# Performance work log

Hardware: AMD Instinct MI355X
Metric: run time of the kernel (lower is better)

The kernel has to match this reference:

```python
import jax, jax.numpy as jnp
import numpy as np

E = 1024          # embed_dim
BUCKET = 16       # bucket_size
TAU = 0.75        # sinkhorn_tau
ITERS = 8         # sinkhorn_iters
SCALE = E ** -0.5


def setup_inputs() -> dict:
    key = jax.random.key(0)
    ks = jax.random.split(key, 12)
    T, S, B = 4096, 4096, 8
    w = 1.0 / np.sqrt(E)  # ~xavier scale
    return {
        "query": jax.random.normal(ks[0], (T, B, E), jnp.float32),
        "key_t": jax.random.normal(ks[1], (S, B, E), jnp.float32),
        "value": jax.random.normal(ks[2], (S, B, E), jnp.float32),
        "key_padding_mask": jnp.zeros((B, S), jnp.bool_),
        "Wq": jax.random.normal(ks[3], (E, E), jnp.float32) * w,
        "bq": jax.random.normal(ks[4], (E,), jnp.float32) * 0.01,
        "Wk": jax.random.normal(ks[5], (E, E), jnp.float32) * w,
        "bk": jax.random.normal(ks[6], (E,), jnp.float32) * 0.01,
        "Wv": jax.random.normal(ks[7], (E, E), jnp.float32) * w,
        "bv": jax.random.normal(ks[8], (E,), jnp.float32) * 0.01,
        "Wo": jax.random.normal(ks[9], (E, E), jnp.float32) * w,
        "bo": jnp.zeros((E,), jnp.float32),
    }


def reference(query, key_t, value, key_padding_mask, Wq, bq, Wk, bk, Wv, bv, Wo, bo):
    # Projections in (T, B, E) layout
    q = query @ Wq.T + bq
    k = key_t @ Wk.T + bk
    v = value @ Wv.T + bv
    # (B, T, E)
    q = jnp.swapaxes(q, 0, 1)
    k = jnp.swapaxes(k, 0, 1)
    v = jnp.swapaxes(v, 0, 1)
    B, T, Ed = q.shape
    S = k.shape[1]
    nb, nkb = T // BUCKET, S // BUCKET  # T,S chosen as exact multiples -> no pad
    # aggregate_buckets: mean-pool q,k; flatten v per bucket
    qb = q.reshape(B, nb, BUCKET, Ed).mean(axis=2)          # (B, nb, E)
    kb = k.reshape(B, nkb, BUCKET, Ed).mean(axis=2)         # (B, nkb, E)
    vb = v.reshape(B, nkb, BUCKET * Ed)                     # (B, nkb, BUCKET*E)
    # key padding mask: bucket is padded iff all positions padded (prod)
    kpm_b = jnp.all(key_padding_mask.reshape(B, nkb, BUCKET), axis=2)  # (B, nkb)
    # energy_fn == 'dot'
    attn = jnp.einsum('bte,bse->bts', qb, kb) * SCALE       # (B, nb, nkb)
    neg_inf = -jnp.finfo(attn.dtype).max
    final_mask = kpm_b[:, None, :] & (~kpm_b)[:, :, None]   # (B, nb, nkb), nb==nkb
    attn = jnp.where(final_mask, neg_inf, attn)
    attn = jnp.where(jnp.swapaxes(final_mask, 1, 2), neg_inf, attn)
    # gumbel_sinkhorn in eval mode (noise_factor=0): log-sinkhorn normalization
    la = attn / TAU
    for _ in range(ITERS):
        la = la - jax.nn.logsumexp(la, axis=-1, keepdims=True)
        la = la - jax.nn.logsumexp(la, axis=-2, keepdims=True)
    p = jnp.exp(la)                                         # (B, nb, nkb)
    # attend over flattened value buckets, then undo bucket aggregation
    out = jnp.einsum('bts,bsf->btf', p, vb)                 # (B, nb, BUCKET*E)
    out = out.reshape(B, nb * BUCKET, Ed)                   # (B, T, E)
    out = jnp.swapaxes(out, 0, 1)                           # (T, B, E)
    return out @ Wo.T + bo
```

## Files before the change

kernel.cpp:

```cpp
#include <hip/hip_runtime.h>


typedef __bf16 bhalf;
typedef __bf16 bh4 __attribute__((ext_vector_type(4)));
typedef __bf16 bh8 __attribute__((ext_vector_type(8)));
typedef float f32x4 __attribute__((ext_vector_type(4)));

__device__ __forceinline__ void async16(const bhalf* g, bhalf* l) {
    __builtin_amdgcn_global_load_lds(
        (const __attribute__((address_space(1))) unsigned int*)g,
        (__attribute__((address_space(3))) unsigned int*)l,
        16, 0, 0);
}

__device__ __forceinline__ void f2b_body(const float* in, bhalf* out, int idx) {
    const float4* p = (const float4*)in + (size_t)idx * 2;
    float4 x = p[0], y = p[1];
    bh8 o;
    o[0] = (bhalf)x.x; o[1] = (bhalf)x.y; o[2] = (bhalf)x.z; o[3] = (bhalf)x.w;
    o[4] = (bhalf)y.x; o[5] = (bhalf)y.y; o[6] = (bhalf)y.z; o[7] = (bhalf)y.w;
    *(bh8*)(out + (size_t)idx * 8) = o;
}

__global__ void f2b_kernel(const float* __restrict__ in, bhalf* __restrict__ out, int n8) {
    int idx = blockIdx.x * 256 + threadIdx.x;
    if (idx < n8) f2b_body(in, out, idx);
}

__global__ void f2b4_kernel(const float* __restrict__ a, const float* __restrict__ b,
                            const float* __restrict__ c, const float* __restrict__ d,
                            bhalf* __restrict__ out) {
    const float* srcs[4] = {a, b, c, d};
    int idx = blockIdx.x * 256 + threadIdx.x;
    f2b_body(srcs[blockIdx.y], out + (size_t)blockIdx.y * 1048576, idx);
}

__global__ void pool2_kernel(const float* __restrict__ q, const float* __restrict__ k,
                             bhalf* __restrict__ oq, bhalf* __restrict__ ok) {
    const float* in = blockIdx.y ? k : q;
    bhalf* out = blockIdx.y ? ok : oq;
    int row = blockIdx.x;
    int b = row >> 8, tb = row & 255;
    int e = threadIdx.x * 4;
    const float* base = in + ((size_t)(tb * 16) * 8 + b) * 1024 + e;
    float sx = 0.f, sy = 0.f, sz = 0.f, sw = 0.f;
#pragma unroll
    for (int i = 0; i < 16; ++i) {
        float4 v = *(const float4*)(base + (size_t)i * 8192);
        sx += v.x; sy += v.y; sz += v.z; sw += v.w;
    }
    bh4 o;
    o[0] = (bhalf)(sx * 0.0625f);
    o[1] = (bhalf)(sy * 0.0625f);
    o[2] = (bhalf)(sz * 0.0625f);
    o[3] = (bhalf)(sw * 0.0625f);
    *(bh4*)(out + (size_t)row * 1024 + e) = o;
}

__global__ __launch_bounds__(256) void gemm_nt(
    const bhalf* __restrict__ A, const bhalf* __restrict__ B,
    void* __restrict__ Cv, const float* __restrict__ bias, const float* __restrict__ bias2,
    int lda, int ldb, long ldc, int K,
    float alpha, int outBf16, int swz,
    long zsA, long zsB, long zsC, unsigned zmaskA)
{
    __shared__ bhalf As[128 * 64];
    __shared__ bhalf Bs[128 * 64];
    unsigned z = blockIdx.z;
    A += (size_t)(z & zmaskA) * zsA;
    B += (size_t)z * zsB;
    if (z == 1 && bias2) bias = bias2;
    long coff = (long)z * zsC;
    int bx = blockIdx.x, by = blockIdx.y;
    if (swz) {
        int linear = by * 8 + bx;
        int xcd = linear & 7, idx = linear >> 3;
        bx = idx & 7;
        by = xcd * ((int)gridDim.y >> 3) + (idx >> 3);
    }
    int m0 = by * 128, n0 = bx * 128;
    int tid = threadIdx.x;
    int w = tid >> 6, lane = tid & 63;
    int quad = lane >> 4, l16 = lane & 15;
    int wm = (w & 1) * 64, wn = (w >> 1) * 64;
    int srow = lane >> 3;
    int sg = (lane & 7) ^ srow;

    f32x4 acc[4][4] = {};

    for (int k0 = 0; k0 < K; k0 += 64) {
#pragma unroll
        for (int j = 0; j < 4; ++j) {
            int blk = j * 4 + w;
            int r = blk * 8 + srow;
            async16(A + (size_t)(m0 + r) * lda + (k0 + sg * 8), &As[blk * 512]);
            async16(B + (size_t)(n0 + r) * ldb + (k0 + sg * 8), &Bs[blk * 512]);
        }
        __syncthreads();
#pragma unroll
        for (int kk = 0; kk < 2; ++kk) {
            bh8 fa[4], fb[4];
            int gsw = (((kk << 2) + quad) ^ (l16 & 7)) * 8;
#pragma unroll
            for (int i = 0; i < 4; ++i) {
                fa[i] = *(const bh8*)&As[(wm + i * 16 + l16) * 64 + gsw];
                fb[i] = *(const bh8*)&Bs[(wn + i * 16 + l16) * 64 + gsw];
            }
#pragma unroll
            for (int i = 0; i < 4; ++i)
#pragma unroll
                for (int j = 0; j < 4; ++j)
                    acc[i][j] = __builtin_amdgcn_mfma_f32_16x16x32_bf16(
                        fa[i], fb[j], acc[i][j], 0, 0, 0);
        }
        __syncthreads();
    }

#pragma unroll
    for (int i = 0; i < 4; ++i) {
        int row = m0 + wm + i * 16 + quad * 4;
#pragma unroll
        for (int j = 0; j < 4; ++j) {
            int col = n0 + wn + j * 16 + l16;
            float bb = bias ? bias[col] : 0.f;
#pragma unroll
            for (int r2 = 0; r2 < 4; ++r2) {
                float v = alpha * acc[i][j][r2] + bb;
                long off = coff + (long)(row + r2) * ldc + col;
                if (outBf16) ((bhalf*)Cv)[off] = (bhalf)v;
                else         ((float*)Cv)[off] = v;
            }
        }
    }
}

__global__ __launch_bounds__(1024) void sinkhorn_kernel(
    const float* __restrict__ la_in, bhalf* __restrict__ p_out)
{
    int b = blockIdx.x;
    const float* A = la_in + (size_t)b * 65536;
    int tid = threadIdx.x;
    int br = tid >> 5, bc = tid & 31;
    int r0 = br * 8, c0 = bc * 8;
    float a[8][8];
#pragma unroll
    for (int r = 0; r < 8; ++r) {
        float4 v0 = *(const float4*)(A + (size_t)(r0 + r) * 256 + c0);
        float4 v1 = *(const float4*)(A + (size_t)(r0 + r) * 256 + c0 + 4);
        a[r][0] = v0.x; a[r][1] = v0.y; a[r][2] = v0.z; a[r][3] = v0.w;
        a[r][4] = v1.x; a[r][5] = v1.y; a[r][6] = v1.z; a[r][7] = v1.w;
    }
    __shared__ float lm[16][256];
    __shared__ float ls[16][256];

    for (int it = 0; it < 8; ++it) {
#pragma unroll
        for (int r = 0; r < 8; ++r) {
            float m = a[r][0];
#pragma unroll
            for (int c = 1; c < 8; ++c) m = fmaxf(m, a[r][c]);
#pragma unroll
            for (int d = 1; d < 32; d <<= 1) m = fmaxf(m, __shfl_xor(m, d, 64));
            float s = 0.f;
#pragma unroll
            for (int c = 0; c < 8; ++c) s += __expf(a[r][c] - m);
#pragma unroll
            for (int d = 1; d < 32; d <<= 1) s += __shfl_xor(s, d, 64);
            float lse = m + __logf(s);
#pragma unroll
            for (int c = 0; c < 8; ++c) a[r][c] -= lse;
        }
        __syncthreads();
#pragma unroll
        for (int c = 0; c < 8; ++c) {
            float m = a[0][c];
#pragma unroll
            for (int r = 1; r < 8; ++r) m = fmaxf(m, a[r][c]);
            float s = 0.f;
#pragma unroll
            for (int r = 0; r < 8; ++r) s += __expf(a[r][c] - m);
            float mo = __shfl_xor(m, 32, 64);
            float so = __shfl_xor(s, 32, 64);
            float M2 = fmaxf(m, mo);
            float S2 = s * __expf(m - M2) + so * __expf(mo - M2);
            if ((br & 1) == 0) { lm[br >> 1][c0 + c] = M2; ls[br >> 1][c0 + c] = S2; }
        }
        __syncthreads();
        if (tid < 256) {
            int col = tid;
            float M = lm[0][col];
#pragma unroll
            for (int j = 1; j < 16; ++j) M = fmaxf(M, lm[j][col]);
            float S = 0.f;
#pragma unroll
            for (int j = 0; j < 16; ++j) S += ls[j][col] * __expf(lm[j][col] - M);
            lm[0][col] = M + __logf(S);
        }
        __syncthreads();
#pragma unroll
        for (int c = 0; c < 8; ++c) {
            float lse = lm[0][c0 + c];
#pragma unroll
            for (int r = 0; r < 8; ++r) a[r][c] -= lse;
        }
    }
#pragma unroll
    for (int r = 0; r < 8; ++r) {
        bh8 o;
#pragma unroll
        for (int c = 0; c < 8; ++c) o[c] = (bhalf)__expf(a[r][c]);
        *(bh8*)(p_out + (size_t)b * 65536 + (size_t)(r0 + r) * 256 + c0) = o;
    }
}

__global__ void transpose_v_kernel(const bhalf* __restrict__ vp, bhalf* __restrict__ vT) {
    int z = blockIdx.x;
    int i = z >> 3, b = z & 7;
    int e0 = blockIdx.y * 64, s0 = blockIdx.z * 64;
    __shared__ bhalf t[64][72];
    for (int g = threadIdx.x; g < 512; g += 256) {
        int r = g >> 3, gc = g & 7;
        size_t row = ((size_t)(s0 + r) * 16 + i) * 8 + b;
        *(uint4*)&t[r][gc * 8] = *(const uint4*)(vp + row * 1024 + e0 + gc * 8);
    }
    __syncthreads();
    for (int g = threadIdx.x; g < 512; g += 256) {
        int er = g >> 3, gc = g & 7;
        bh8 o;
#pragma unroll
        for (int j = 0; j < 8; ++j) o[j] = t[gc * 8 + j][er];
        *(bh8*)(vT + (size_t)z * 262144 + (size_t)(e0 + er) * 256 + (s0 + gc * 8)) = o;
    }
}

extern "C" void kernel_launch(void* const* d_in, const int* in_sizes, int n_in,
                              void* d_out, int out_size, void* d_ws, size_t ws_size,
                              hipStream_t stream) {
    const float* query = (const float*)d_in[0];
    const float* key_t = (const float*)d_in[1];
    const float* value = (const float*)d_in[2];
    const float* Wq = (const float*)d_in[4];
    const float* bq = (const float*)d_in[5];
    const float* Wk = (const float*)d_in[6];
    const float* bk = (const float*)d_in[7];
    const float* Wv = (const float*)d_in[8];
    const float* bv = (const float*)d_in[9];
    const float* Wo = (const float*)d_in[10];
    const float* bo = (const float*)d_in[11];

    char* ws = (char*)d_ws;
    bhalf* val_bf = (bhalf*)(ws);
    bhalf* vT     = val_bf;
    bhalf* vproj  = (bhalf*)(ws + 67108864);
    bhalf* outp   = vproj;
    bhalf* Wq_b   = (bhalf*)(ws + 134217728);
    bhalf* Wk_b   = Wq_b + 1048576;
    bhalf* Wv_b   = Wk_b + 1048576;
    bhalf* Wo_b   = Wv_b + 1048576;
    bhalf* qp     = Wo_b + 1048576;
    bhalf* kp     = qp + 2097152;
    bhalf* qbp    = kp + 2097152;
    bhalf* kbp    = qbp + 2097152;
    float* la     = (float*)(kbp + 2097152);
    bhalf* p_bf   = (bhalf*)(la + 524288);

    const float SCALE_TAU = (1.0f / 32.0f) / 0.75f;
    const unsigned ALLZ = 0xffffffffu;

    f2b4_kernel<<<dim3(512, 4), 256, 0, stream>>>(Wq, Wk, Wv, Wo, Wq_b);
    f2b_kernel<<<16384, 256, 0, stream>>>(value, val_bf, 4194304);

    pool2_kernel<<<dim3(2048, 2), 256, 0, stream>>>(query, key_t, qp, kp);

    gemm_nt<<<dim3(8, 16, 2), 256, 0, stream>>>(qp, Wq_b, qbp, bq, bk,
        1024, 1024, 1024, 1024, 1.0f, 1, 0, 2097152, 1048576, 2097152, ALLZ);

    gemm_nt<<<dim3(2, 2, 8), 256, 0, stream>>>(qbp, kbp, la, nullptr, nullptr,
        1024, 1024, 256, 1024, SCALE_TAU, 0, 0, 262144, 262144, 65536, ALLZ);

    sinkhorn_kernel<<<8, 1024, 0, stream>>>(la, p_bf);

    gemm_nt<<<dim3(8, 256, 1), 256, 0, stream>>>(val_bf, Wv_b, vproj, bv, nullptr,
        1024, 1024, 1024, 1024, 1.0f, 1, 1, 0, 0, 0, 0u);

    transpose_v_kernel<<<dim3(128, 16, 4), 256, 0, stream>>>(vproj, vT);

    gemm_nt<<<dim3(8, 2, 128), 256, 0, stream>>>(p_bf, vT, outp, nullptr, nullptr,
        256, 256, 131072, 256, 1.0f, 1, 0, 65536, 262144, 1024, 7u);

    gemm_nt<<<dim3(8, 256, 1), 256, 0, stream>>>(outp, Wo_b, (float*)d_out, bo, nullptr,
        1024, 1024, 1024, 1024, 1.0f, 0, 1, 0, 0, 0, 0u);
}
```

Baseline: 776.2 us.

## Add 256x256-tile double-buffered GEMM for value and output projections

Adds a new gemm256 kernel with 256x256 output tiles, 512 threads, a double-buffered async global-to-LDS pipeline, an XOR-swizzled LDS layout, setprio around the MFMA bursts and XCD-aware block remapping. The two large 32768x1024x1024 projections (value and output) move from the 128x128-tile gemm_nt to this kernel, aiming for more operand reuse and better overlap of loads with MFMA work. The larger tiles use 128 KB of LDS per block and many accumulator registers, which may limit occupancy.

```diff
diff --git a/kernel.cpp b/kernel.cpp
--- a/kernel.cpp
+++ b/kernel.cpp
@@ -127,6 +127,106 @@
             for (int r2 = 0; r2 < 4; ++r2) {
                 float v = alpha * acc[i][j][r2] + bb;
                 long off = coff + (long)(row + r2) * ldc + col;
+                if (outBf16) ((bhalf*)Cv)[off] = (bhalf)v;
+                else         ((float*)Cv)[off] = v;
+            }
+        }
+    }
+}
+
+__device__ __forceinline__ void stage256(const bhalf* __restrict__ A,
+                                         const bhalf* __restrict__ B,
+                                         bhalf* as, bhalf* bs,
+                                         int m0, int n0, int lda, int ldb,
+                                         int k0, int w, int lane)
+{
+    int r8 = lane >> 3;
+    int colb = k0 + (((lane & 7) ^ r8) << 3);
+    const bhalf* ap = A + (size_t)(m0 + w * 8 + r8) * lda + colb;
+    const bhalf* bp = B + (size_t)(n0 + w * 8 + r8) * ldb + colb;
+    bhalf* asw = as + w * 512;
+    bhalf* bsw = bs + w * 512;
+#pragma unroll
+    for (int s = 0; s < 4; ++s) {
+        async16(ap + (size_t)(s * 64) * lda, asw + s * 4096);
+        async16(bp + (size_t)(s * 64) * ldb, bsw + s * 4096);
+    }
+}
+
+__device__ __forceinline__ void compute256(const bhalf* as, const bhalf* bs,
+                                           int wr, int wc, int quad, int l16,
+                                           f32x4 (&acc)[8][4])
+{
+#pragma unroll
+    for (int kk = 0; kk < 2; ++kk) {
+        bh8 fa[8], fb[4];
+        int gsw = (((kk << 2) + quad) ^ (l16 & 7)) << 3;
+#pragma unroll
+        for (int i = 0; i < 8; ++i)
+            fa[i] = *(const bh8*)&as[(wr * 128 + i * 16 + l16) * 64 + gsw];
+#pragma unroll
+        for (int j = 0; j < 4; ++j)
+            fb[j] = *(const bh8*)&bs[(wc * 64 + j * 16 + l16) * 64 + gsw];
+        __builtin_amdgcn_s_setprio(1);
+#pragma unroll
+        for (int i = 0; i < 8; ++i)
+#pragma unroll
+            for (int j = 0; j < 4; ++j)
+                acc[i][j] = __builtin_amdgcn_mfma_f32_16x16x32_bf16(
+                    fa[i], fb[j], acc[i][j], 0, 0, 0);
+        __builtin_amdgcn_s_setprio(0);
+    }
+}
+
+__global__ __launch_bounds__(512, 2) void gemm256(
+    const bhalf* __restrict__ A, const bhalf* __restrict__ B,
+    void* __restrict__ Cv, const float* __restrict__ bias,
+    int K, int outBf16)
+{
+    __shared__ __align__(16) bhalf As[2][16384];
+    __shared__ __align__(16) bhalf Bs[2][16384];
+
+    int nx = (int)gridDim.x;
+    int linear = blockIdx.y * nx + blockIdx.x;
+    int xcd = linear & 7, idx = linear >> 3;
+    int bx = idx % nx;
+    int by = xcd * ((int)gridDim.y >> 3) + idx / nx;
+    int m0 = by << 8, n0 = bx << 8;
+
+    int tid = threadIdx.x;
+    int w = tid >> 6, lane = tid & 63;
+    int quad = lane >> 4, l16 = lane & 15;
+    int wr = w & 1, wc = w >> 1;
+    const int lda = K, ldb = K;
+
+    f32x4 acc[8][4] = {};
+    int nt = K >> 6;
+
+    stage256(A, B, As[0], Bs[0], m0, n0, lda, ldb, 0, w, lane);
+    for (int t = 0; t < nt - 1; ++t) {
+        stage256(A, B, As[(t + 1) & 1], Bs[(t + 1) & 1], m0, n0, lda, ldb,
+                 (t + 1) << 6, w, lane);
+        asm volatile("s_waitcnt vmcnt(8)" ::: "memory");
+        asm volatile("s_barrier" ::: "memory");
+        compute256(As[t & 1], Bs[t & 1], wr, wc, quad, l16, acc);
+        asm volatile("s_barrier" ::: "memory");
+    }
+    asm volatile("s_waitcnt vmcnt(0)" ::: "memory");
+    asm volatile("s_barrier" ::: "memory");
+    compute256(As[(nt - 1) & 1], Bs[(nt - 1) & 1], wr, wc, quad, l16, acc);
+
+    const long ldc = 1024;
+#pragma unroll
+    for (int i = 0; i < 8; ++i) {
+        int row = m0 + wr * 128 + i * 16 + quad * 4;
+#pragma unroll
+        for (int j = 0; j < 4; ++j) {
+            int col = n0 + wc * 64 + j * 16 + l16;
+            float bb = bias[col];
+#pragma unroll
+            for (int r2 = 0; r2 < 4; ++r2) {
+                float v = acc[i][j][r2] + bb;
+                long off = (long)(row + r2) * ldc + col;
                 if (outBf16) ((bhalf*)Cv)[off] = (bhalf)v;
                 else         ((float*)Cv)[off] = v;
             }
@@ -280,14 +380,12 @@
 
     sinkhorn_kernel<<<8, 1024, 0, stream>>>(la, p_bf);
 
-    gemm_nt<<<dim3(8, 256, 1), 256, 0, stream>>>(val_bf, Wv_b, vproj, bv, nullptr,
-        1024, 1024, 1024, 1024, 1.0f, 1, 1, 0, 0, 0, 0u);
+    gemm256<<<dim3(4, 128), 512, 0, stream>>>(val_bf, Wv_b, vproj, bv, 1024, 1);
 
     transpose_v_kernel<<<dim3(128, 16, 4), 256, 0, stream>>>(vproj, vT);
 
     gemm_nt<<<dim3(8, 2, 128), 256, 0, stream>>>(p_bf, vT, outp, nullptr, nullptr,
         256, 256, 131072, 256, 1.0f, 1, 0, 65536, 262144, 1024, 7u);
 
-    gemm_nt<<<dim3(8, 256, 1), 256, 0, stream>>>(outp, Wo_b, (float*)d_out, bo, nullptr,
-        1024, 1024, 1024, 1024, 1.0f, 0, 1, 0, 0, 0, 0u);
-}
+    gemm256<<<dim3(4, 128), 512, 0, stream>>>(outp, Wo_b, (float*)d_out, bo, 1024, 0);
+}
```

Result: no change. 770.5 us (-0.7%).
